# Performance work log

Hardware: AMD Instinct MI355X
Metric: run time of the kernel (lower is better)

The kernel has to match this reference:

```python
import jax, jax.numpy as jnp
import numpy as np

DIM = 256
HEADS = 8
SEQ = 4096
SCALE = DIM ** -0.5  # note: original scales by full dim, not head dim


def setup_inputs() -> dict:
    key = jax.random.key(0)
    ks = jax.random.split(key, 5)
    x = jax.random.normal(ks[0], (SEQ, DIM), dtype=jnp.float32)
    w_qkv = jax.random.normal(ks[1], (DIM, 3 * DIM), dtype=jnp.float32) * (DIM ** -0.5)
    b_qkv = jnp.zeros((3 * DIM,), dtype=jnp.float32)
    w_out = jax.random.normal(ks[2], (DIM, DIM), dtype=jnp.float32) * (DIM ** -0.5)
    b_out = jnp.zeros((DIM,), dtype=jnp.float32)
    return {"x": x, "w_qkv": w_qkv, "b_qkv": b_qkv, "w_out": w_out, "b_out": b_out}


def reference(x, w_qkv, b_qkv, w_out, b_out):
    n, dim = x.shape
    h = HEADS
    d = dim // h
    qkv = x @ w_qkv + b_qkv                      # [n, 3*dim]
    q, k, v = jnp.split(qkv, 3, axis=-1)         # each [n, dim]
    # 'n (h d) -> h n d'
    q = q.reshape(n, h, d).transpose(1, 0, 2)
    k = k.reshape(n, h, d).transpose(1, 0, 2)
    v = v.reshape(n, h, d).transpose(1, 0, 2)
    dots = jnp.einsum('hid,hjd->hij', q, k) * SCALE  # [h, n, n]
    attn = jax.nn.softmax(dots, axis=-1)
    out = jnp.einsum('hij,hjd->hid', attn, v)        # [h, n, d]
    out = out.transpose(1, 0, 2).reshape(n, dim)     # 'h n d -> n (h d)'
    return out @ w_out + b_out                       # [n, dim]
```

## Files before the change

kernel.cpp:

```cpp
#include <hip/hip_runtime.h>
#include <stdint.h>

#define SEQ   4096
#define DIM   256
#define HDIM  32
#define HEADS 8
#define W3    768
#define LOG2E 1.4426950408889634f

typedef float  f32x4  __attribute__((ext_vector_type(4)));
typedef float  f32x2  __attribute__((ext_vector_type(2)));
typedef float  fl4    __attribute__((ext_vector_type(4)));
typedef short  bf16x8 __attribute__((ext_vector_type(8)));
typedef short  bf16x4 __attribute__((ext_vector_type(4)));

static __device__ __forceinline__ f32x4 MFMA_PV(bf16x4 a, bf16x4 b, f32x4 c) {
#if defined(__HIP_DEVICE_COMPILE__)
# if __has_builtin(__builtin_amdgcn_mfma_f32_16x16x16_bf16)
    return __builtin_amdgcn_mfma_f32_16x16x16_bf16(a, b, c, 0, 0, 0);
# elif __has_builtin(__builtin_amdgcn_mfma_f32_16x16x16bf16_1k)
    return __builtin_amdgcn_mfma_f32_16x16x16bf16_1k(a, b, c, 0, 0, 0);
# else
    f32x4 d;
    asm volatile("v_mfma_f32_16x16x16_bf16 %0, %1, %2, %3"
                 : "=v"(d) : "v"(a), "v"(b), "v"(c));
    return d;
# endif
#else
    (void)a; (void)b;
    return c;
#endif
}

__device__ __forceinline__ unsigned short f2bf(float f) {
    union { __bf16 h; unsigned short u; } v;
    v.h = (__bf16)f;
    return v.u;
}
__device__ __forceinline__ short f2bf_s(float f) {
    union { __bf16 h; short s; } v;
    v.h = (__bf16)f;
    return v.s;
}

__global__ __launch_bounds__(256) void prep_kernel(
    const float* __restrict__ x, const float* __restrict__ wqkv,
    const float* __restrict__ wout,
    unsigned short* __restrict__ xb,
    unsigned short* __restrict__ wt,
    unsigned short* __restrict__ wot)
{
    __shared__ float lds[64][65];
    const int b   = blockIdx.x;
    const int tid = threadIdx.x;
    if (b < 64) {
        const float* src;
        unsigned short* dst;
        int N, i0, j0;
        if (b < 48) {
            src = wqkv; dst = wt; N = W3;
            i0 = (b & 3) * 64; j0 = (b >> 2) * 64;
        } else {
            int bb = b - 48;
            src = wout; dst = wot; N = DIM;
            i0 = (bb & 3) * 64; j0 = (bb >> 2) * 64;
        }
        const int c = tid & 63, grp = tid >> 6;
        #pragma unroll
        for (int k = 0; k < 16; ++k) {
            int r = grp * 16 + k;
            lds[r][c] = src[(size_t)(i0 + r) * N + j0 + c];
        }
        __syncthreads();
        #pragma unroll
        for (int k = 0; k < 16; ++k) {
            int cc = grp * 16 + k;
            dst[(size_t)(j0 + cc) * DIM + i0 + c] = f2bf(lds[c][cc]);
        }
    } else {
        const fl4* __restrict__ x4 = (const fl4*)x;
        const int total4 = SEQ * DIM / 4;
        for (int i = (b - 64) * 256 + tid; i < total4; i += 64 * 256) {
            fl4 v = x4[i];
            ushort4 o;
            o.x = f2bf(v[0]); o.y = f2bf(v[1]);
            o.z = f2bf(v[2]); o.w = f2bf(v[3]);
            *reinterpret_cast<ushort4*>(xb + (size_t)i * 4) = o;
        }
    }
}

__global__ __launch_bounds__(256) void qkv_gemm(
    const unsigned short* __restrict__ xb,
    const unsigned short* __restrict__ wt,
    const float* __restrict__ bqkv,
    unsigned short* __restrict__ Qb,
    unsigned short* __restrict__ Kb,
    unsigned short* __restrict__ Vb)
{
    const int wid  = threadIdx.x >> 6;
    const int lane = threadIdx.x & 63;
    const int g    = lane >> 4, li = lane & 15;
    const int row0 = blockIdx.x * 64 + wid * 16;
    const int col0 = blockIdx.y * 64;

    f32x4 acc[4];
    #pragma unroll
    for (int c = 0; c < 4; ++c)
        acc[c] = (f32x4){0.f, 0.f, 0.f, 0.f};

    #pragma unroll
    for (int ks = 0; ks < DIM; ks += 32) {
        bf16x8 a = *(const bf16x8*)(xb + (size_t)(row0 + li) * DIM + ks + g * 8);
        bf16x8 b[4];
        #pragma unroll
        for (int c = 0; c < 4; ++c)
            b[c] = *(const bf16x8*)(wt + (size_t)(col0 + 16 * c + li) * DIM + ks + g * 8);
        #pragma unroll
        for (int c = 0; c < 4; ++c)
            acc[c] = __builtin_amdgcn_mfma_f32_16x16x32_bf16(a, b[c], acc[c], 0, 0, 0);
    }

    #pragma unroll
    for (int c = 0; c < 4; ++c)
        #pragma unroll
        for (int r = 0; r < 4; ++r) {
            int row = row0 + g * 4 + r;
            int col = col0 + 16 * c + li;
            float v = acc[c][r] + bqkv[col];
            int sec = col >> 8;
            int cc  = col & 255;
            int hh  = cc >> 5, dd = cc & 31;
            if (sec == 0)
                Qb[((size_t)hh * SEQ + row) * HDIM + dd] = f2bf(v * (0.0625f * LOG2E));
            else if (sec == 1)
                Kb[((size_t)hh * SEQ + row) * HDIM + dd] = f2bf(v);
            else
                Vb[(size_t)hh * SEQ * HDIM + ((size_t)(row >> 4) * HDIM + dd) * 16 + (row & 15)] = f2bf(v);
        }
}

__global__ __launch_bounds__(256) void attn_kernel(
    const unsigned short* __restrict__ Qb,
    const unsigned short* __restrict__ Kb,
    const unsigned short* __restrict__ Vb,
    float* __restrict__ Opart,
    float* __restrict__ Lp,
    int nc)
{
    __shared__ float obuf[2][32 * 64];
    __shared__ float lbuf[2][4 * 64];
    const int wid  = threadIdx.x >> 6;
    const int lane = threadIdx.x & 63;
    const int g    = lane >> 4, li = lane & 15;
    const int head = blockIdx.y;
    const int chunk = blockIdx.z;
    const int qs   = wid & 1;
    const int half = wid >> 1;
    const int r0   = blockIdx.x * 128 + qs * 64;
    const int span  = SEQ / nc;
    const int wspan = span >> 1;
    const int jb0   = chunk * span + half * wspan;
    const int ntile = wspan / 64;

    const unsigned short* Qh = Qb + (size_t)head * SEQ * HDIM;
    const unsigned short* kp = Kb + (size_t)head * SEQ * HDIM + (size_t)jb0 * HDIM
                             + (size_t)li * HDIM + g * 8;
    const unsigned short* vp = Vb + (size_t)head * SEQ * HDIM + (size_t)jb0 * HDIM
                             + (size_t)li * 16 + 4 * g;

    bf16x8 aq[4];
    #pragma unroll
    for (int t = 0; t < 4; ++t)
        aq[t] = *(const bf16x8*)(Qh + (size_t)(r0 + 16 * t + li) * HDIM + g * 8);

    f32x4 o[4][2];
    #pragma unroll
    for (int t = 0; t < 4; ++t)
        #pragma unroll
        for (int nt = 0; nt < 2; ++nt)
            o[t][nt] = (f32x4){0.f, 0.f, 0.f, 0.f};
    f32x2 lacc2[4];
    #pragma unroll
    for (int t = 0; t < 4; ++t)
        lacc2[t] = (f32x2){0.f, 0.f};

    const f32x4 zero4 = (f32x4){0.f, 0.f, 0.f, 0.f};

    for (int it = 0; it < ntile; ++it) {
        bf16x8 bk[4];
        #pragma unroll
        for (int c = 0; c < 4; ++c)
            bk[c] = *(const bf16x8*)(kp + c * (16 * HDIM));
        bf16x4 bv[4][2];
        #pragma unroll
        for (int c = 0; c < 4; ++c)
            #pragma unroll
            for (int nt = 0; nt < 2; ++nt)
                bv[c][nt] = *(const bf16x4*)(vp + c * (16 * HDIM) + nt * 256);

        #pragma unroll
        for (int c = 0; c < 4; ++c) {
            #pragma unroll
            for (int t = 0; t < 4; ++t) {
                f32x4 s = __builtin_amdgcn_mfma_f32_16x16x32_bf16(bk[c], aq[t], zero4, 0, 0, 0);
                float p0 = __builtin_amdgcn_exp2f(s[0]);
                float p1 = __builtin_amdgcn_exp2f(s[1]);
                float p2 = __builtin_amdgcn_exp2f(s[2]);
                float p3 = __builtin_amdgcn_exp2f(s[3]);
                f32x2 ps; ps[0] = p0 + p2; ps[1] = p1 + p3;
                lacc2[t] += ps;
                bf16x4 pa;
                pa[0] = f2bf_s(p0); pa[1] = f2bf_s(p1);
                pa[2] = f2bf_s(p2); pa[3] = f2bf_s(p3);
                o[t][0] = MFMA_PV(pa, bv[c][0], o[t][0]);
                o[t][1] = MFMA_PV(pa, bv[c][1], o[t][1]);
            }
        }
        kp += 2048; vp += 2048;
    }

    if (half == 1) {
        #pragma unroll
        for (int t = 0; t < 4; ++t)
            #pragma unroll
            for (int nt = 0; nt < 2; ++nt)
                #pragma unroll
                for (int r = 0; r < 4; ++r)
                    obuf[qs][((t * 2 + nt) * 4 + r) * 64 + lane] = o[t][nt][r];
        #pragma unroll
        for (int t = 0; t < 4; ++t)
            lbuf[qs][t * 64 + lane] = lacc2[t][0] + lacc2[t][1];
    }
    __syncthreads();
    if (half == 1) return;

    float lacc[4];
    #pragma unroll
    for (int t = 0; t < 4; ++t) {
        #pragma unroll
        for (int nt = 0; nt < 2; ++nt)
            #pragma unroll
            for (int r = 0; r < 4; ++r)
                o[t][nt][r] += obuf[qs][((t * 2 + nt) * 4 + r) * 64 + lane];
        lacc[t] = lacc2[t][0] + lacc2[t][1] + lbuf[qs][t * 64 + lane];
    }

    #pragma unroll
    for (int t = 0; t < 4; ++t) {
        float L = lacc[t];
        L += __shfl_xor(L, 16);
        L += __shfl_xor(L, 32);
        lacc[t] = L;
    }

    float* Oc = Opart + (size_t)chunk * SEQ * DIM;
    #pragma unroll
    for (int t = 0; t < 4; ++t)
        #pragma unroll
        for (int nt = 0; nt < 2; ++nt)
            #pragma unroll
            for (int r = 0; r < 4; ++r) {
                int row = r0 + 16 * t + g * 4 + r;
                int col = head * HDIM + 16 * nt + li;
                Oc[(size_t)row * DIM + col] = o[t][nt][r];
            }
    if (lane < 16) {
        #pragma unroll
        for (int t = 0; t < 4; ++t) {
            int row = r0 + 16 * t + lane;
            Lp[((size_t)chunk * HEADS + head) * SEQ + row] = lacc[t];
        }
    }
}

__global__ __launch_bounds__(256) void combine_kernel(
    const float* __restrict__ Opart, const float* __restrict__ Lp,
    unsigned short* __restrict__ AO, int nc)
{
    int idx = blockIdx.x * 256 + threadIdx.x;
    int row = idx >> 6;
    int cp  = (idx & 63) << 2;
    int head = cp >> 5;
    float L = 0.f;
    fl4 a = (fl4){0.f, 0.f, 0.f, 0.f};
    for (int i = 0; i < nc; ++i) {
        L += Lp[((size_t)i * HEADS + head) * SEQ + row];
        a += *(const fl4*)(Opart + (size_t)i * SEQ * DIM + (size_t)row * DIM + cp);
    }
    float inv = 1.f / L;
    ushort4 pk;
    pk.x = f2bf(a[0] * inv); pk.y = f2bf(a[1] * inv);
    pk.z = f2bf(a[2] * inv); pk.w = f2bf(a[3] * inv);
    *reinterpret_cast<ushort4*>(AO + (size_t)row * DIM + cp) = pk;
}

__global__ __launch_bounds__(256) void out_gemm(
    const unsigned short* __restrict__ AO,
    const unsigned short* __restrict__ wot,
    const float* __restrict__ bout,
    float* __restrict__ out)
{
    const int wid  = threadIdx.x >> 6;
    const int lane = threadIdx.x & 63;
    const int g    = lane >> 4, li = lane & 15;
    const int row0 = blockIdx.x * 64 + wid * 16;
    const int col0 = blockIdx.y * 64;

    f32x4 acc[4];
    #pragma unroll
    for (int c = 0; c < 4; ++c)
        acc[c] = (f32x4){0.f, 0.f, 0.f, 0.f};

    #pragma unroll
    for (int ks = 0; ks < DIM; ks += 32) {
        bf16x8 a = *(const bf16x8*)(AO + (size_t)(row0 + li) * DIM + ks + g * 8);
        bf16x8 b[4];
        #pragma unroll
        for (int c = 0; c < 4; ++c)
            b[c] = *(const bf16x8*)(wot + (size_t)(col0 + 16 * c + li) * DIM + ks + g * 8);
        #pragma unroll
        for (int c = 0; c < 4; ++c)
            acc[c] = __builtin_amdgcn_mfma_f32_16x16x32_bf16(a, b[c], acc[c], 0, 0, 0);
    }

    #pragma unroll
    for (int c = 0; c < 4; ++c)
        #pragma unroll
        for (int r = 0; r < 4; ++r) {
            int row = row0 + g * 4 + r;
            int col = col0 + 16 * c + li;
            out[(size_t)row * DIM + col] = acc[c][r] + bout[col];
        }
}

extern "C" void kernel_launch(void* const* d_in, const int* in_sizes, int n_in,
                              void* d_out, int out_size, void* d_ws, size_t ws_size,
                              hipStream_t stream)
{
    const float* x    = (const float*)d_in[0];
    const float* wqkv = (const float*)d_in[1];
    const float* bqkv = (const float*)d_in[2];
    const float* wout = (const float*)d_in[3];
    const float* bout = (const float*)d_in[4];
    float* out = (float*)d_out;

    char* ws = (char*)d_ws;
    const size_t OFF_XB  = 0;
    const size_t OFF_WT  = 2097152;
    const size_t OFF_WOT = 2490368;
    const size_t OFF_QB  = 2621440;
    const size_t OFF_KB  = 4718592;
    const size_t OFF_VT  = 6815744;
    const size_t OFF_AO  = 8912896;
    const size_t OFF_OP  = 11010048;
    const size_t OP_CH   = (size_t)SEQ * DIM * 4;
    const size_t LP_CH   = (size_t)HEADS * SEQ * 4;

    int nc = 4;
    while (nc > 1 && OFF_OP + (size_t)nc * (OP_CH + LP_CH) > ws_size) nc >>= 1;
    if (OFF_OP + (size_t)nc * (OP_CH + LP_CH) > ws_size) return;

    unsigned short* xb  = (unsigned short*)(ws + OFF_XB);
    unsigned short* wt  = (unsigned short*)(ws + OFF_WT);
    unsigned short* wot = (unsigned short*)(ws + OFF_WOT);
    unsigned short* Qb  = (unsigned short*)(ws + OFF_QB);
    unsigned short* Kb  = (unsigned short*)(ws + OFF_KB);
    unsigned short* Vb  = (unsigned short*)(ws + OFF_VT);
    unsigned short* AO  = (unsigned short*)(ws + OFF_AO);
    float* Opart = (float*)(ws + OFF_OP);
    float* Lp    = (float*)(ws + OFF_OP + (size_t)nc * OP_CH);

    hipLaunchKernelGGL(prep_kernel, dim3(128), dim3(256), 0, stream,
                       x, wqkv, wout, xb, wt, wot);
    hipLaunchKernelGGL(qkv_gemm, dim3(64, 12), dim3(256), 0, stream,
                       xb, wt, bqkv, Qb, Kb, Vb);
    hipLaunchKernelGGL(attn_kernel, dim3(SEQ / 128, HEADS, nc), dim3(256), 0, stream,
                       Qb, Kb, Vb, Opart, Lp, nc);
    hipLaunchKernelGGL(combine_kernel, dim3(SEQ * DIM / 1024), dim3(256), 0, stream,
                       Opart, Lp, AO, nc);
    hipLaunchKernelGGL(out_gemm, dim3(SEQ / 64, DIM / 64), dim3(256), 0, stream,
                       AO, wot, bout, out);
}
```

Before: 72.52 us.

## Stage K/V tiles in double-buffered LDS and fuse combine into output GEMM

The attention kernel now has all four waves share one key/value range, staged through double-buffered shared memory, in place of splitting keys between wave pairs and reducing through LDS. Each block covers 256 query rows, and the key split grows from 4 to 8 chunks. The separate combine kernel is removed. The output GEMM sums the partial outputs, normalises them and converts to bf16 on the fly, saving one launch and the AO round trip. The cost is a barrier every tile in attention and more partial-output reads in the output GEMM, where each row's partials are read by four waves.

```diff
diff --git a/kernel.cpp b/kernel.cpp
--- a/kernel.cpp
+++ b/kernel.cpp
@@ -148,26 +148,22 @@
     float* __restrict__ Lp,
     int nc)
 {
-    __shared__ float obuf[2][32 * 64];
-    __shared__ float lbuf[2][4 * 64];
-    const int wid  = threadIdx.x >> 6;
-    const int lane = threadIdx.x & 63;
+    __shared__ unsigned short Kst[2][2048];
+    __shared__ unsigned short Vst[2][2048];
+    const int tid  = threadIdx.x;
+    const int wid  = tid >> 6;
+    const int lane = tid & 63;
     const int g    = lane >> 4, li = lane & 15;
     const int head = blockIdx.y;
     const int chunk = blockIdx.z;
-    const int qs   = wid & 1;
-    const int half = wid >> 1;
-    const int r0   = blockIdx.x * 128 + qs * 64;
+    const int r0   = blockIdx.x * 256 + wid * 64;
     const int span  = SEQ / nc;
-    const int wspan = span >> 1;
-    const int jb0   = chunk * span + half * wspan;
-    const int ntile = wspan / 64;
+    const int jb0   = chunk * span;
+    const int ntile = span / 64;
 
     const unsigned short* Qh = Qb + (size_t)head * SEQ * HDIM;
-    const unsigned short* kp = Kb + (size_t)head * SEQ * HDIM + (size_t)jb0 * HDIM
-                             + (size_t)li * HDIM + g * 8;
-    const unsigned short* vp = Vb + (size_t)head * SEQ * HDIM + (size_t)jb0 * HDIM
-                             + (size_t)li * 16 + 4 * g;
+    const unsigned short* Kg = Kb + (size_t)head * SEQ * HDIM + (size_t)jb0 * HDIM + tid * 8;
+    const unsigned short* Vg = Vb + (size_t)head * SEQ * HDIM + (size_t)jb0 * HDIM + tid * 8;
 
     bf16x8 aq[4];
     #pragma unroll
@@ -187,17 +183,32 @@
 
     const f32x4 zero4 = (f32x4){0.f, 0.f, 0.f, 0.f};
 
+    {
+        bf16x8 kreg = *(const bf16x8*)(Kg);
+        bf16x8 vreg = *(const bf16x8*)(Vg);
+        *(bf16x8*)&Kst[0][tid * 8] = kreg;
+        *(bf16x8*)&Vst[0][tid * 8] = vreg;
+    }
+    __syncthreads();
+
+    int cur = 0;
     for (int it = 0; it < ntile; ++it) {
+        bf16x8 kreg, vreg;
+        if (it + 1 < ntile) {
+            kreg = *(const bf16x8*)(Kg + (size_t)(it + 1) * 2048);
+            vreg = *(const bf16x8*)(Vg + (size_t)(it + 1) * 2048);
+        }
+
         bf16x8 bk[4];
         #pragma unroll
         for (int c = 0; c < 4; ++c)
-            bk[c] = *(const bf16x8*)(kp + c * (16 * HDIM));
+            bk[c] = *(const bf16x8*)&Kst[cur][(16 * c + li) * 32 + 8 * g];
         bf16x4 bv[4][2];
         #pragma unroll
         for (int c = 0; c < 4; ++c)
             #pragma unroll
             for (int nt = 0; nt < 2; ++nt)
-                bv[c][nt] = *(const bf16x4*)(vp + c * (16 * HDIM) + nt * 256);
+                bv[c][nt] = *(const bf16x4*)&Vst[cur][c * 512 + (16 * nt + li) * 16 + 4 * g];
 
         #pragma unroll
         for (int c = 0; c < 4; ++c) {
@@ -217,38 +228,19 @@
                 o[t][1] = MFMA_PV(pa, bv[c][1], o[t][1]);
             }
         }
-        kp += 2048; vp += 2048;
-    }
-
-    if (half == 1) {
-        #pragma unroll
-        for (int t = 0; t < 4; ++t)
-            #pragma unroll
-            for (int nt = 0; nt < 2; ++nt)
-                #pragma unroll
-                for (int r = 0; r < 4; ++r)
-                    obuf[qs][((t * 2 + nt) * 4 + r) * 64 + lane] = o[t][nt][r];
-        #pragma unroll
-        for (int t = 0; t < 4; ++t)
-            lbuf[qs][t * 64 + lane] = lacc2[t][0] + lacc2[t][1];
-    }
-    __syncthreads();
-    if (half == 1) return;
+
+        if (it + 1 < ntile) {
+            *(bf16x8*)&Kst[cur ^ 1][tid * 8] = kreg;
+            *(bf16x8*)&Vst[cur ^ 1][tid * 8] = vreg;
+        }
+        __syncthreads();
+        cur ^= 1;
+    }
 
     float lacc[4];
     #pragma unroll
     for (int t = 0; t < 4; ++t) {
-        #pragma unroll
-        for (int nt = 0; nt < 2; ++nt)
-            #pragma unroll
-            for (int r = 0; r < 4; ++r)
-                o[t][nt][r] += obuf[qs][((t * 2 + nt) * 4 + r) * 64 + lane];
-        lacc[t] = lacc2[t][0] + lacc2[t][1] + lbuf[qs][t * 64 + lane];
-    }
-
-    #pragma unroll
-    for (int t = 0; t < 4; ++t) {
-        float L = lacc[t];
+        float L = lacc2[t][0] + lacc2[t][1];
         L += __shfl_xor(L, 16);
         L += __shfl_xor(L, 32);
         lacc[t] = L;
@@ -274,38 +266,18 @@
     }
 }
 
-__global__ __launch_bounds__(256) void combine_kernel(
+__global__ __launch_bounds__(256) void out_gemm(
     const float* __restrict__ Opart, const float* __restrict__ Lp,
-    unsigned short* __restrict__ AO, int nc)
-{
-    int idx = blockIdx.x * 256 + threadIdx.x;
-    int row = idx >> 6;
-    int cp  = (idx & 63) << 2;
-    int head = cp >> 5;
-    float L = 0.f;
-    fl4 a = (fl4){0.f, 0.f, 0.f, 0.f};
-    for (int i = 0; i < nc; ++i) {
-        L += Lp[((size_t)i * HEADS + head) * SEQ + row];
-        a += *(const fl4*)(Opart + (size_t)i * SEQ * DIM + (size_t)row * DIM + cp);
-    }
-    float inv = 1.f / L;
-    ushort4 pk;
-    pk.x = f2bf(a[0] * inv); pk.y = f2bf(a[1] * inv);
-    pk.z = f2bf(a[2] * inv); pk.w = f2bf(a[3] * inv);
-    *reinterpret_cast<ushort4*>(AO + (size_t)row * DIM + cp) = pk;
-}
-
-__global__ __launch_bounds__(256) void out_gemm(
-    const unsigned short* __restrict__ AO,
     const unsigned short* __restrict__ wot,
     const float* __restrict__ bout,
-    float* __restrict__ out)
+    float* __restrict__ out, int nc)
 {
     const int wid  = threadIdx.x >> 6;
     const int lane = threadIdx.x & 63;
     const int g    = lane >> 4, li = lane & 15;
-    const int row0 = blockIdx.x * 64 + wid * 16;
-    const int col0 = blockIdx.y * 64;
+    const int row0 = blockIdx.x * 16;
+    const int col0 = wid * 64;
+    const int arow = row0 + li;
 
     f32x4 acc[4];
     #pragma unroll
@@ -314,7 +286,23 @@
 
     #pragma unroll
     for (int ks = 0; ks < DIM; ks += 32) {
-        bf16x8 a = *(const bf16x8*)(AO + (size_t)(row0 + li) * DIM + ks + g * 8);
+        const int hh = ks >> 5;
+        fl4 a0 = (fl4){0.f, 0.f, 0.f, 0.f};
+        fl4 a1 = (fl4){0.f, 0.f, 0.f, 0.f};
+        float L = 0.f;
+        for (int i = 0; i < nc; ++i) {
+            const float* p = Opart + (size_t)i * SEQ * DIM + (size_t)arow * DIM + ks + g * 8;
+            a0 += *(const fl4*)p;
+            a1 += *(const fl4*)(p + 4);
+            L  += Lp[((size_t)i * HEADS + hh) * SEQ + arow];
+        }
+        float inv = 1.f / L;
+        bf16x8 a;
+        #pragma unroll
+        for (int e = 0; e < 4; ++e) {
+            a[e]     = f2bf_s(a0[e] * inv);
+            a[4 + e] = f2bf_s(a1[e] * inv);
+        }
         bf16x8 b[4];
         #pragma unroll
         for (int c = 0; c < 4; ++c)
@@ -352,12 +340,11 @@
     const size_t OFF_QB  = 2621440;
     const size_t OFF_KB  = 4718592;
     const size_t OFF_VT  = 6815744;
-    const size_t OFF_AO  = 8912896;
     const size_t OFF_OP  = 11010048;
     const size_t OP_CH   = (size_t)SEQ * DIM * 4;
     const size_t LP_CH   = (size_t)HEADS * SEQ * 4;
 
-    int nc = 4;
+    int nc = 8;
     while (nc > 1 && OFF_OP + (size_t)nc * (OP_CH + LP_CH) > ws_size) nc >>= 1;
     if (OFF_OP + (size_t)nc * (OP_CH + LP_CH) > ws_size) return;
 
@@ -367,7 +354,6 @@
     unsigned short* Qb  = (unsigned short*)(ws + OFF_QB);
     unsigned short* Kb  = (unsigned short*)(ws + OFF_KB);
     unsigned short* Vb  = (unsigned short*)(ws + OFF_VT);
-    unsigned short* AO  = (unsigned short*)(ws + OFF_AO);
     float* Opart = (float*)(ws + OFF_OP);
     float* Lp    = (float*)(ws + OFF_OP + (size_t)nc * OP_CH);
 
@@ -375,10 +361,8 @@
                        x, wqkv, wout, xb, wt, wot);
     hipLaunchKernelGGL(qkv_gemm, dim3(64, 12), dim3(256), 0, stream,
                        xb, wt, bqkv, Qb, Kb, Vb);
-    hipLaunchKernelGGL(attn_kernel, dim3(SEQ / 128, HEADS, nc), dim3(256), 0, stream,
+    hipLaunchKernelGGL(attn_kernel, dim3(SEQ / 256, HEADS, nc), dim3(256), 0, stream,
                        Qb, Kb, Vb, Opart, Lp, nc);
-    hipLaunchKernelGGL(combine_kernel, dim3(SEQ * DIM / 1024), dim3(256), 0, stream,
-                       Opart, Lp, AO, nc);
-    hipLaunchKernelGGL(out_gemm, dim3(SEQ / 64, DIM / 64), dim3(256), 0, stream,
-                       AO, wot, bout, out);
-}
+    hipLaunchKernelGGL(out_gemm, dim3(SEQ / 16), dim3(256), 0, stream,
+                       Opart, Lp, wot, bout, out, nc);
+}
```

After: 90.51 us. 24.8% more time.
